# Kernel optimization log

Hardware: AMD Instinct MI355X
Metric: run time of the kernel (lower is better)

Reference implementation:

```python
import jax, jax.numpy as jnp
import numpy as np

B, T, D = 2, 2048, 2048
N, K, H = 16, 8, 128            # heads, kv heads, head_dim
SOFT_CAP = 50.0
WINDOW = 1024
SCALE = H ** -0.5               # query_pre_attn_scalar
ROPE_BASE = 10000.0
ROPE_SCALE = 1.0
K_MASK = -2.3819763e+38


def rms_norm(x, scale, eps=1e-6):
    var = jnp.mean(jnp.square(x), axis=-1, keepdims=True)
    return x * jax.lax.rsqrt(var + eps) * (1.0 + scale)


def apply_rope(x, positions):
    # x: [B,T,heads,H]; positions: [B,T] int
    head_dim = x.shape[-1]
    fraction = 2.0 * jnp.arange(head_dim // 2, dtype=jnp.float32) / head_dim
    timescale = ROPE_BASE ** fraction                      # [H/2]
    sinusoid = positions[..., None].astype(jnp.float32) / timescale  # [B,T,H/2]
    sinusoid = sinusoid[..., None, :] / ROPE_SCALE          # [B,T,1,H/2]
    sin, cos = jnp.sin(sinusoid), jnp.cos(sinusoid)
    first, second = jnp.split(x, 2, axis=-1)
    return jnp.concatenate([first * cos - second * sin,
                            second * cos + first * sin], axis=-1)


def setup_inputs() -> dict:
    key = jax.random.key(0)
    ks = jax.random.split(key, 6)
    x = jax.random.normal(ks[0], (B, T, D), jnp.float32)
    q_w = jax.random.normal(ks[1], (N, D, H), jnp.float32) * (D ** -0.5)
    kv_w = jax.random.normal(ks[2], (2, K, D, H), jnp.float32) * (D ** -0.5)
    o_w = jax.random.normal(ks[3], (N, H, D), jnp.float32) * ((N * H) ** -0.5)
    qnorm_scale = 0.1 * jax.random.normal(ks[4], (H,), jnp.float32)
    knorm_scale = 0.1 * jax.random.normal(ks[5], (H,), jnp.float32)
    segment_pos = jnp.broadcast_to(jnp.arange(T, dtype=jnp.int32), (B, T))
    attn_mask = jnp.broadcast_to(jnp.tril(jnp.ones((T, T), dtype=bool)), (B, T, T))
    return {"x": x, "q_w": q_w, "kv_w": kv_w, "o_w": o_w,
            "qnorm_scale": qnorm_scale, "knorm_scale": knorm_scale,
            "segment_pos": segment_pos, "attn_mask": attn_mask}


def reference(x, q_w, kv_w, o_w, qnorm_scale, knorm_scale, segment_pos, attn_mask):
    # projections
    q = jnp.einsum('BTD,NDH->BTNH', x, q_w)            # [B,T,N,H]
    k = jnp.einsum('BSD,KDH->BSKH', x, kv_w[0])        # [B,T,K,H]
    v = jnp.einsum('BSD,KDH->BSKH', x, kv_w[1])
    # QK RMSNorm, then RoPE, then query scaling (matches source order)
    q = apply_rope(rms_norm(q, qnorm_scale), segment_pos) * SCALE
    k = apply_rope(rms_norm(k, knorm_scale), segment_pos)
    # GQA: regroup query heads per kv head
    G = N // K
    qg = q.reshape(B, T, K, G, H)
    logits = jnp.einsum('BTKGH,BSKH->BTKGS', qg, k).reshape(B, T, N, T)
    # logit soft cap
    logits = jnp.tanh(logits / SOFT_CAP) * SOFT_CAP
    # sliding window mask combined with causal attn_mask
    pos_q = segment_pos[:, :, None]
    pos_k = segment_pos[:, None, :]
    sliding = (pos_k > pos_q - WINDOW) & (pos_k < pos_q + WINDOW)
    mask = attn_mask & sliding                          # [B,T,S]
    padded = jnp.where(mask[:, :, None, :], logits, K_MASK)
    probs = jax.nn.softmax(padded, axis=-1).astype(k.dtype)
    enc = jnp.einsum('BTKGS,BSKH->BTKGH',
                     probs.reshape(B, T, K, G, T), v).reshape(B, T, N, H)
    return jnp.einsum('BTNH,NHD->BTD', enc, o_w)
```

## Files before the change

kernel.cpp:

```cpp
#include <hip/hip_runtime.h>
#include <stdint.h>

#define BB 2
#define TT 2048
#define DD 2048
#define NHD 16
#define KVH 8
#define HD 128
#define JC 4096
#define WIN 1024
#define SCALE_Q 0.08838834764831845f

typedef __attribute__((ext_vector_type(8))) short bf16x8;
typedef __attribute__((ext_vector_type(8))) unsigned short us8;
typedef __attribute__((ext_vector_type(4))) unsigned short us4;
typedef __attribute__((ext_vector_type(4))) float f32x4;
typedef __attribute__((ext_vector_type(16))) float f32x16;
typedef __attribute__((ext_vector_type(4))) unsigned int u32x4;

#define GAS __attribute__((address_space(1)))
#define LAS __attribute__((address_space(3)))

__device__ __forceinline__ unsigned short f2bf(float f) {
  unsigned u = __float_as_uint(f);
  u += 0x7FFFu + ((u >> 16) & 1u);
  return (unsigned short)(u >> 16);
}
__device__ __forceinline__ float bf2f(unsigned short u) {
  return __uint_as_float(((unsigned)u) << 16);
}

__device__ __forceinline__ void gload16(const void* g, void* l) {
  __builtin_amdgcn_global_load_lds((const GAS unsigned int*)g, (LAS unsigned int*)l, 16, 0, 0);
}

#define VMCNT(n) asm volatile("s_waitcnt vmcnt(" #n ")" ::: "memory")

__global__ void __launch_bounds__(256) k_cvt(const float4* __restrict__ in,
                                             us4* __restrict__ out, int n4) {
  int i = blockIdx.x * 256 + threadIdx.x;
  if (i >= n4) return;
  float4 v = in[i];
  us4 o;
  o[0] = f2bf(v.x); o[1] = f2bf(v.y); o[2] = f2bf(v.z); o[3] = f2bf(v.w);
  out[i] = o;
}

__global__ void __launch_bounds__(256) k_transpose_cvt(
    const float* __restrict__ in, unsigned short* __restrict__ out,
    int R, int C, int ldin, long b0s, int nbi, long b1s, long obs) {
  __shared__ float tile[32][33];
  int z = blockIdx.z;
  const float* ib = in + (long)(z / nbi) * b0s + (long)(z % nbi) * b1s;
  unsigned short* ob = out + (long)z * obs;
  int c0 = blockIdx.x * 32, r0 = blockIdx.y * 32;
  int tx = threadIdx.x, ty = threadIdx.y;
#pragma unroll
  for (int i = 0; i < 4; i++)
    tile[ty + i * 8][tx] = ib[(long)(r0 + ty + i * 8) * ldin + c0 + tx];
  __syncthreads();
#pragma unroll
  for (int i = 0; i < 4; i++)
    ob[(long)(c0 + ty + i * 8) * R + r0 + tx] = f2bf(tile[tx][ty + i * 8]);
}

__global__ void __launch_bounds__(256) k_wt(const float* __restrict__ qw,
                                            const float* __restrict__ kvw,
                                            unsigned short* __restrict__ out) {
  __shared__ float tile[32][33];
  int z = blockIdx.z;
  const float* ib = (z < 16) ? qw + (long)z * 2048 * 128 : kvw + (long)(z - 16) * 2048 * 128;
  unsigned short* ob = out + (long)z * 128 * 2048;
  int c0 = blockIdx.x * 32, r0 = blockIdx.y * 32;
  int tx = threadIdx.x, ty = threadIdx.y;
#pragma unroll
  for (int i = 0; i < 4; i++)
    tile[ty + i * 8][tx] = ib[(long)(r0 + ty + i * 8) * 128 + c0 + tx];
  __syncthreads();
#pragma unroll
  for (int i = 0; i < 4; i++)
    ob[(long)(c0 + ty + i * 8) * 2048 + r0 + tx] = f2bf(tile[tx][ty + i * 8]);
}

__global__ void __launch_bounds__(256) k_transpose_bf(
    const unsigned short* __restrict__ in, unsigned short* __restrict__ out,
    int R, int C, int ldin, long b0s, int nbi, long b1s, long obs) {
  __shared__ unsigned short tile[32][33];
  int z = blockIdx.z;
  const unsigned short* ib = in + (long)(z / nbi) * b0s + (long)(z % nbi) * b1s;
  unsigned short* ob = out + (long)z * obs;
  int c0 = blockIdx.x * 32, r0 = blockIdx.y * 32;
  int tx = threadIdx.x, ty = threadIdx.y;
#pragma unroll
  for (int i = 0; i < 4; i++)
    tile[ty + i * 8][tx] = ib[(long)(r0 + ty + i * 8) * ldin + c0 + tx];
  __syncthreads();
#pragma unroll
  for (int i = 0; i < 4; i++)
    ob[(long)(c0 + ty + i * 8) * R + r0 + tx] = tile[tx][ty + i * 8];
}

template <int BM, int BN, int NWN, int THREADS, int NBUF, bool BF16OUT>
__global__ void __launch_bounds__(THREADS, 2) k_gemm9(
    const unsigned short* __restrict__ A, const unsigned short* __restrict__ Bt,
    void* __restrict__ Cv, int M, int Nn, int nby) {
  constexpr int KD = 2048;
  constexpr int NT = KD / 32;
  constexpr int ROWS = BM + BN;
  constexpr int RPI = THREADS / 4;
  constexpr int IA = BM / RPI;
  constexpr int IPT = ROWS / RPI;
  constexpr int MT = 8, MT2 = 4;
  __shared__ short lds[NBUF][ROWS * 32];

  int tid = threadIdx.x, lane = tid & 63, w = tid >> 6;
  int wm = w / NWN, wn = w % NWN;
  int id = blockIdx.x;
  int cpx = gridDim.x >> 3;
  id = (id & 7) * cpx + (id >> 3);
  int m0 = (id / nby) * BM, n0 = (id % nby) * BN;

  int srow = tid >> 2;
  int scol = ((tid & 3) ^ ((tid >> 3) & 3)) * 8;
  const unsigned short* gA = A + (long)(m0 + srow) * KD + scol;
  const unsigned short* gB = Bt + (long)(n0 + srow) * KD + scol;

  auto STG = [&](int p, int ko, int j) {
    if (j < IA)
      gload16(gA + (long)j * RPI * KD + ko, &lds[p][(j * RPI + w * 16) * 32]);
    else
      gload16(gB + (long)(j - IA) * RPI * KD + ko,
              &lds[p][(BM + (j - IA) * RPI + w * 16) * 32]);
  };

  int frag = (lane & 15) * 32 + (((lane >> 4) ^ ((lane >> 1) & 3)) * 8);
  int abase = wm * 128 * 32 + frag;
  int bbase = (BM + wn * 64) * 32 + frag;

  f32x4 acc[MT][4] = {};
#pragma unroll
  for (int tt = 0; tt < NBUF - 1; ++tt)
#pragma unroll
    for (int j = 0; j < IPT; ++j) STG(tt, tt * 32, j);
  if constexpr (IPT * (NBUF - 2) == 8) VMCNT(8);
  else VMCNT(6);
  __builtin_amdgcn_s_barrier();

  int buf = 0, sp = NBUF - 1;
  for (int t = 0; t < NT; ++t) {
    const short* bufp = lds[buf];
    bool st = (t + NBUF - 1) < NT;
    int ko = (t + NBUF - 1) * 32;
    bf16x8 bfr[4], af[MT2];
#pragma unroll
    for (int ni = 0; ni < 4; ++ni)
      bfr[ni] = *(const bf16x8*)&bufp[bbase + ni * 16 * 32];
#pragma unroll
    for (int mi = 0; mi < MT2; ++mi)
      af[mi] = *(const bf16x8*)&bufp[abase + mi * 16 * 32];
    if (st) {
#pragma unroll
      for (int j = 0; j < IPT / 2; ++j) STG(sp, ko, j);
    }
    __builtin_amdgcn_s_barrier();
    asm volatile("s_waitcnt lgkmcnt(0)" ::: "memory");
    __builtin_amdgcn_sched_barrier(0);
    __builtin_amdgcn_s_setprio(1);
#pragma unroll
    for (int mi = 0; mi < MT2; ++mi)
#pragma unroll
      for (int ni = 0; ni < 4; ++ni)
        acc[mi][ni] = __builtin_amdgcn_mfma_f32_16x16x32_bf16(af[mi], bfr[ni], acc[mi][ni], 0, 0, 0);
    __builtin_amdgcn_s_setprio(0);
    __builtin_amdgcn_s_barrier();
    bf16x8 af2[MT2];
#pragma unroll
    for (int mi = 0; mi < MT2; ++mi)
      af2[mi] = *(const bf16x8*)&bufp[abase + (MT2 + mi) * 16 * 32];
    if (st) {
#pragma unroll
      for (int j = IPT / 2; j < IPT; ++j) STG(sp, ko, j);
    }
    {
      int rem = NT - 2 - t;
      if (rem > NBUF - 2) rem = NBUF - 2;
      if (rem == 2) {
        if constexpr (IPT == 4) VMCNT(8); else VMCNT(12);
      } else if (rem == 1) {
        if constexpr (IPT == 4) VMCNT(4); else VMCNT(6);
      } else if (rem == 0) {
        VMCNT(0);
      }
    }
    __builtin_amdgcn_s_barrier();
    asm volatile("s_waitcnt lgkmcnt(0)" ::: "memory");
    __builtin_amdgcn_sched_barrier(0);
    __builtin_amdgcn_s_setprio(1);
#pragma unroll
    for (int mi = 0; mi < MT2; ++mi)
#pragma unroll
      for (int ni = 0; ni < 4; ++ni)
        acc[MT2 + mi][ni] = __builtin_amdgcn_mfma_f32_16x16x32_bf16(af2[mi], bfr[ni], acc[MT2 + mi][ni], 0, 0, 0);
    __builtin_amdgcn_s_setprio(0);
    __builtin_amdgcn_s_barrier();
    buf = (buf == NBUF - 1) ? 0 : buf + 1;
    sp = (sp == NBUF - 1) ? 0 : sp + 1;
  }

#pragma unroll
  for (int mi = 0; mi < MT; mi++)
#pragma unroll
    for (int ni = 0; ni < 4; ni++)
#pragma unroll
      for (int r = 0; r < 4; r++) {
        int row = m0 + wm * 128 + mi * 16 + (lane >> 4) * 4 + r;
        int col = n0 + wn * 64 + ni * 16 + (lane & 15);
        if constexpr (BF16OUT)
          ((unsigned short*)Cv)[(long)row * Nn + col] = f2bf(acc[mi][ni][r]);
        else
          ((float*)Cv)[(long)row * Nn + col] = acc[mi][ni][r];
      }
}

__global__ void __launch_bounds__(256) k_norm_rope(
    const unsigned short* __restrict__ qkv, const float* __restrict__ qns,
    const float* __restrict__ kns,
    unsigned short* __restrict__ qb, unsigned short* __restrict__ kb) {
  int wid = threadIdx.x >> 6, lane = threadIdx.x & 63;
  long r = (long)blockIdx.x * 4 + wid;
  int b = (int)(r / (TT * 24));
  int rem = (int)(r % (TT * 24));
  int t = rem / 24, hd = rem % 24;
  const unsigned short* row = qkv + (long)(b * TT + t) * JC + (hd < 16 ? hd * HD : 2048 + (hd - 16) * HD);
  float f0 = bf2f(row[lane]), f1 = bf2f(row[lane + 64]);
  float ss = f0 * f0 + f1 * f1;
#pragma unroll
  for (int m = 1; m < 64; m <<= 1) ss += __shfl_xor(ss, m, 64);
  float rinv = rsqrtf(ss * (1.0f / 128.0f) + 1e-6f);
  const float* sc = (hd < 16) ? qns : kns;
  float y0 = f0 * rinv * (1.0f + sc[lane]);
  float y1 = f1 * rinv * (1.0f + sc[lane + 64]);
  float ts = exp2f((float)lane * (13.287712379549449f / 64.0f));
  float ang = (float)t / ts;
  float s, c;
  sincosf(ang, &s, &c);
  float o0 = y0 * c - y1 * s;
  float o1 = y1 * c + y0 * s;
  unsigned short* dst;
  if (hd < 16) {
    o0 *= SCALE_Q; o1 *= SCALE_Q;
    dst = qb + ((long)(b * NHD + hd) * TT + t) * HD;
  } else {
    dst = kb + ((long)(b * KVH + (hd - 16)) * TT + t) * HD;
  }
  dst[lane] = f2bf(o0);
  dst[lane + 64] = f2bf(o1);
}

template <bool FULL>
__device__ __forceinline__ void softcap16(const f32x16& s16, float* pr, float& lsum,
                                          int s_base, int tq, int g) {
#pragma unroll
  for (int r = 0; r < 16; r++) {
    float x = s16[r];
    float e = __builtin_amdgcn_exp2f(-0.05770780163555853f * fabsf(x));
    float u = (x > 0.0f ? e : 1.0f) * __builtin_amdgcn_rcpf(1.0f + e);
    float p = __builtin_amdgcn_exp2f(-144.26950408889634f * u);
    if (!FULL) {
      int s = s_base + (r & 3) + 8 * (r >> 2) + 4 * g;
      bool valid = (s <= tq) && (s > tq - WIN);
      p = valid ? p : 0.0f;
    }
    lsum += p;
    pr[r] = p;
  }
}

__device__ __forceinline__ void hswap(unsigned& a, unsigned& b, int g) {
  unsigned ax = (unsigned)__shfl_xor((int)a, 32, 64);
  unsigned bx = (unsigned)__shfl_xor((int)b, 32, 64);
  unsigned r0 = g ? bx : a;
  unsigned r1 = g ? b : ax;
  a = r0; b = r1;
}

__global__ void __launch_bounds__(256, 2) k_attn(
    const unsigned short* __restrict__ qb, const unsigned short* __restrict__ kb,
    const unsigned short* __restrict__ vbT, unsigned short* __restrict__ enc) {
  __shared__ short Kl[2][64][128];
  __shared__ short Vt[2][128][64];
  int tid = threadIdx.x, lane = tid & 63, w = tid >> 6;
  int g = lane >> 5, l31 = lane & 31;
  int id = blockIdx.x;
  int b = id >> 8;
  int rem = id & 255;
  int n = rem >> 4;
  int traw = rem & 15;
  int tile = b ? ((traw + 8) & 15) : traw;
  int t0 = tile * 128;
  int kh = n >> 1;
  const unsigned short* qbase = qb + ((long)(b * NHD + n) * TT + t0 + w * 32) * HD;
  const unsigned short* kbase = kb + (long)(b * KVH + kh) * TT * HD;
  const unsigned short* vbase = vbT + (long)(b * KVH + kh) * HD * TT;

  bf16x8 bq[8];
  {
    const unsigned short* qp = qbase + (long)l31 * HD + g * 8;
#pragma unroll
    for (int kb8 = 0; kb8 < 8; kb8++)
      bq[kb8] = *(const bf16x8*)(qp + kb8 * 16);
  }

  f32x16 acc[4] = {};
  float lsum = 0.0f;
  int t0w = t0 + w * 32;
  int tq = t0w + l31;
  int s_begin = (t0 >= WIN) ? t0 - WIN : 0;
  int s_end = t0 + 128;

  auto STAGE = [&](int buf, int s0) {
#pragma unroll
    for (int i = 0; i < 4; i++) {
      int row = w * 16 + i * 4 + (lane >> 4);
      int c16 = (lane & 15) ^ (row & 7);
      gload16(kbase + (long)(s0 + row) * HD + c16 * 8, &Kl[buf][w * 16 + i * 4][0]);
    }
#pragma unroll
    for (int i = 0; i < 4; i++) {
      int row = w * 32 + i * 8 + (lane >> 3);
      int c16 = (lane & 7) ^ (row & 7);
      gload16(vbase + (long)row * TT + s0 + c16 * 8, &Vt[buf][w * 32 + i * 8][0]);
    }
  };

  STAGE(0, s_begin);
  __syncthreads();
  int cur = 0;
  for (int s0 = s_begin; s0 < s_end; s0 += 64) {
    if (s0 + 64 < s_end) STAGE(cur ^ 1, s0 + 64);
    bool live = (s0 <= t0w + 31) && (s0 + 63 >= t0w - (WIN - 1));
    if (live) {
      f32x16 sc2[2] = {};
#pragma unroll
      for (int sb = 0; sb < 2; sb++) {
        int srow = sb * 32 + l31;
#pragma unroll
        for (int kb8 = 0; kb8 < 8; kb8++) {
          bf16x8 ak = *(const bf16x8*)&Kl[cur][srow][8 * ((2 * kb8 + g) ^ (srow & 7))];
          sc2[sb] = __builtin_amdgcn_mfma_f32_32x32x16_bf16(ak, bq[kb8], sc2[sb], 0, 0, 0);
        }
      }
      bool full = (s0 + 63 <= t0w) && (s0 >= t0w + 31 - (WIN - 1));
      unsigned pw[4][4];
#pragma unroll
      for (int sb = 0; sb < 2; sb++) {
        float pr[16];
        if (full) softcap16<true>(sc2[sb], pr, lsum, 0, tq, g);
        else      softcap16<false>(sc2[sb], pr, lsum, s0 + sb * 32, tq, g);
        unsigned X[4], Y[4];
#pragma unroll
        for (int m = 0; m < 4; m++) {
          asm("v_cvt_pk_bf16_f32 %0, %1, %2" : "=v"(X[m]) : "v"(pr[4 * m]), "v"(pr[4 * m + 1]));
          asm("v_cvt_pk_bf16_f32 %0, %1, %2" : "=v"(Y[m]) : "v"(pr[4 * m + 2]), "v"(pr[4 * m + 3]));
        }
#pragma unroll
        for (int kl = 0; kl < 2; kl++) {
          hswap(X[2 * kl], X[2 * kl + 1], g);
          hswap(Y[2 * kl], Y[2 * kl + 1], g);
          pw[sb * 2 + kl][0] = X[2 * kl];
          pw[sb * 2 + kl][1] = Y[2 * kl];
          pw[sb * 2 + kl][2] = X[2 * kl + 1];
          pw[sb * 2 + kl][3] = Y[2 * kl + 1];
        }
      }
#pragma unroll
      for (int ks = 0; ks < 4; ks++) {
        u32x4 t4 = {pw[ks][0], pw[ks][1], pw[ks][2], pw[ks][3]};
        bf16x8 pb = __builtin_bit_cast(bf16x8, t4);
#pragma unroll
        for (int ht = 0; ht < 4; ht++) {
          int hrow = ht * 32 + l31;
          bf16x8 av = *(const bf16x8*)&Vt[cur][hrow][8 * ((2 * ks + g) ^ (hrow & 7))];
          acc[ht] = __builtin_amdgcn_mfma_f32_32x32x16_bf16(av, pb, acc[ht], 0, 0, 0);
        }
      }
    }
    __syncthreads();
    cur ^= 1;
  }

  lsum += __shfl_xor(lsum, 32, 64);
  float inv = __builtin_amdgcn_rcpf(lsum);
  unsigned short* dst = enc + ((long)(b * TT + tq) * NHD + n) * HD;
#pragma unroll
  for (int ht = 0; ht < 4; ht++)
#pragma unroll
    for (int r4 = 0; r4 < 4; r4++) {
      us4 o;
#pragma unroll
      for (int e = 0; e < 4; e++) o[e] = f2bf(acc[ht][r4 * 4 + e] * inv);
      *(us4*)(dst + ht * 32 + 8 * r4 + 4 * g) = o;
    }
}

extern "C" void kernel_launch(void* const* d_in, const int* in_sizes, int n_in,
                              void* d_out, int out_size, void* d_ws, size_t ws_size,
                              hipStream_t stream) {
  const float* x    = (const float*)d_in[0];
  const float* q_w  = (const float*)d_in[1];
  const float* kv_w = (const float*)d_in[2];
  const float* o_w  = (const float*)d_in[3];
  const float* qns  = (const float*)d_in[4];
  const float* kns  = (const float*)d_in[5];

  if (ws_size < (104ull << 20)) return;
  char* ws = (char*)d_ws;
  unsigned short* qkvb = (unsigned short*)(ws + 0);
  unsigned short* enc  = (unsigned short*)(ws + 0);
  unsigned short* x_bf = (unsigned short*)(ws + (64ll << 20));
  unsigned short* qb   = (unsigned short*)(ws + (64ll << 20));
  unsigned short* Wt   = (unsigned short*)(ws + (80ll << 20));
  unsigned short* kb   = (unsigned short*)(ws + (80ll << 20));
  unsigned short* vbT  = (unsigned short*)(ws + (88ll << 20));
  unsigned short* Wt_o = (unsigned short*)(ws + (96ll << 20));

  dim3 tb(32, 8, 1);
  k_cvt<<<8192, 256, 0, stream>>>((const float4*)x, (us4*)x_bf, 2097152);
  k_wt<<<dim3(4, 64, 32), tb, 0, stream>>>(q_w, kv_w, Wt);
  k_transpose_cvt<<<dim3(64, 64, 1), tb, 0, stream>>>(o_w, Wt_o, 2048, 2048, 2048, 0, 1, 0, 0);
  k_gemm9<256, 256, 4, 512, 4, true><<<256, 512, 0, stream>>>(x_bf, Wt, qkvb, 4096, 4096, 16);
  k_transpose_bf<<<dim3(4, 64, 16), tb, 0, stream>>>(qkvb + 3072, vbT, 2048, 128, 4096,
                                                     (long)2048 * 4096, 8, 128, (long)128 * 2048);
  k_norm_rope<<<24576, 256, 0, stream>>>(qkvb, qns, kns, qb, kb);
  k_attn<<<512, 256, 0, stream>>>(qb, kb, vbT, enc);
  k_gemm9<256, 128, 2, 256, 3, false><<<256, 256, 0, stream>>>(enc, Wt_o, (float*)d_out, 4096, 2048, 16);
}
```

Before: 224.9 us.

## Merge weight transposes, simplify softcap math, retile QKV projection GEMM

Merges the two weight transpose-convert kernels into a single launch that picks its source by block index, saving one kernel launch. Rewrites the softcapped exponent using one exp2 of the signed logit plus a reciprocal, dropping the abs and select, which relies on exp2 not overflowing for capped logits. Switches the QKV GEMM from 256x256 tiles with 512 threads to 256x128 tiles with 256 threads and 512 blocks, trading per-block reuse for more blocks across the CUs.

```diff
diff --git a/kernel.cpp b/kernel.cpp
--- a/kernel.cpp
+++ b/kernel.cpp
@@ -46,36 +46,30 @@
   out[i] = o;
 }
 
-__global__ void __launch_bounds__(256) k_transpose_cvt(
-    const float* __restrict__ in, unsigned short* __restrict__ out,
-    int R, int C, int ldin, long b0s, int nbi, long b1s, long obs) {
+__global__ void __launch_bounds__(256) k_prep(
+    const float* __restrict__ qw, const float* __restrict__ kvw,
+    const float* __restrict__ ow, unsigned short* __restrict__ Wt,
+    unsigned short* __restrict__ Wt_o) {
   __shared__ float tile[32][33];
-  int z = blockIdx.z;
-  const float* ib = in + (long)(z / nbi) * b0s + (long)(z % nbi) * b1s;
-  unsigned short* ob = out + (long)z * obs;
-  int c0 = blockIdx.x * 32, r0 = blockIdx.y * 32;
+  int id = blockIdx.x;
+  const float* ib;
+  unsigned short* ob;
+  int ldin, c0, r0;
+  if (id < 8192) {
+    int bx = id & 3, by = (id >> 2) & 63, z = id >> 8;
+    ib = (z < 16) ? qw + (long)z * 2048 * 128 : kvw + (long)(z - 16) * 2048 * 128;
+    ob = Wt + (long)z * 128 * 2048;
+    ldin = 128;
+    c0 = bx * 32; r0 = by * 32;
+  } else {
+    int t = id - 8192;
+    ib = ow; ob = Wt_o; ldin = 2048;
+    c0 = (t & 63) * 32; r0 = (t >> 6) * 32;
+  }
   int tx = threadIdx.x, ty = threadIdx.y;
 #pragma unroll
   for (int i = 0; i < 4; i++)
     tile[ty + i * 8][tx] = ib[(long)(r0 + ty + i * 8) * ldin + c0 + tx];
-  __syncthreads();
-#pragma unroll
-  for (int i = 0; i < 4; i++)
-    ob[(long)(c0 + ty + i * 8) * R + r0 + tx] = f2bf(tile[tx][ty + i * 8]);
-}
-
-__global__ void __launch_bounds__(256) k_wt(const float* __restrict__ qw,
-                                            const float* __restrict__ kvw,
-                                            unsigned short* __restrict__ out) {
-  __shared__ float tile[32][33];
-  int z = blockIdx.z;
-  const float* ib = (z < 16) ? qw + (long)z * 2048 * 128 : kvw + (long)(z - 16) * 2048 * 128;
-  unsigned short* ob = out + (long)z * 128 * 2048;
-  int c0 = blockIdx.x * 32, r0 = blockIdx.y * 32;
-  int tx = threadIdx.x, ty = threadIdx.y;
-#pragma unroll
-  for (int i = 0; i < 4; i++)
-    tile[ty + i * 8][tx] = ib[(long)(r0 + ty + i * 8) * 128 + c0 + tx];
   __syncthreads();
 #pragma unroll
   for (int i = 0; i < 4; i++)
@@ -263,9 +257,8 @@
 #pragma unroll
   for (int r = 0; r < 16; r++) {
     float x = s16[r];
-    float e = __builtin_amdgcn_exp2f(-0.05770780163555853f * fabsf(x));
-    float u = (x > 0.0f ? e : 1.0f) * __builtin_amdgcn_rcpf(1.0f + e);
-    float p = __builtin_amdgcn_exp2f(-144.26950408889634f * u);
+    float e2 = __builtin_amdgcn_exp2f(0.05770780163555853f * x);
+    float p = __builtin_amdgcn_exp2f(-144.26950408889634f * __builtin_amdgcn_rcpf(1.0f + e2));
     if (!FULL) {
       int s = s_base + (r & 3) + 8 * (r >> 2) + 4 * g;
       bool valid = (s <= tq) && (s > tq - WIN);
@@ -426,9 +419,8 @@
 
   dim3 tb(32, 8, 1);
   k_cvt<<<8192, 256, 0, stream>>>((const float4*)x, (us4*)x_bf, 2097152);
-  k_wt<<<dim3(4, 64, 32), tb, 0, stream>>>(q_w, kv_w, Wt);
-  k_transpose_cvt<<<dim3(64, 64, 1), tb, 0, stream>>>(o_w, Wt_o, 2048, 2048, 2048, 0, 1, 0, 0);
-  k_gemm9<256, 256, 4, 512, 4, true><<<256, 512, 0, stream>>>(x_bf, Wt, qkvb, 4096, 4096, 16);
+  k_prep<<<12288, tb, 0, stream>>>(q_w, kv_w, o_w, Wt, Wt_o);
+  k_gemm9<256, 128, 2, 256, 3, true><<<512, 256, 0, stream>>>(x_bf, Wt, qkvb, 4096, 4096, 32);
   k_transpose_bf<<<dim3(4, 64, 16), tb, 0, stream>>>(qkvb + 3072, vbT, 2048, 128, 4096,
                                                      (long)2048 * 4096, 8, 128, (long)128 * 2048);
   k_norm_rope<<<24576, 256, 0, stream>>>(qkvb, qns, kns, qb, kb);
```

After: 223.0 us. No clear change (-0.8%).
